# Optimization experiments

Hardware: AMD Instinct MI355X
Metric: run time of the kernel (lower is better)

Reference implementation:

```python
import jax, jax.numpy as jnp
import numpy as np

N = 100000        # num_nodes
E = 3200000       # num_edges
IN_C = 256        # in_channels (feature dim)
OUT_C = 128       # out_channels (embedding dim)
KAPPA = 0.95


def proj_norm_inf(W, kappa):
    """Row-wise projection of W onto the l-inf operator-norm ball of radius kappa:
    rows whose l1 norm exceeds kappa are projected (abs values onto the simplex
    of radius kappa via sort, signs restored). Matches projection_norm_inf."""
    a = jnp.abs(W)
    s = jnp.sign(W)
    rowsum = a.sum(axis=-1)                      # [rows]
    n = W.shape[-1]
    u = jnp.sort(a, axis=-1)[:, ::-1]            # descending
    css = jnp.cumsum(u, axis=-1) - kappa
    ind = jnp.arange(1, n + 1, dtype=W.dtype)
    cond = (u - css / ind) > 0                   # prefix-true pattern
    rho = jnp.sum(cond, axis=-1)                 # number of active coords (>=1 when rowsum>kappa)
    rho_safe = jnp.maximum(rho, 1)
    theta = jnp.take_along_axis(css, (rho_safe - 1)[:, None], axis=-1)[:, 0] / rho_safe.astype(W.dtype)
    w_proj = jnp.maximum(a - theta[:, None], 0.0) * s
    return jnp.where((rowsum > kappa)[:, None], w_proj, W)


def gcn_conv(x, W, src, dst, num_nodes):
    """PyG GCNConv (bias=False, normalize=True, add_self_loops=True):
    out = D^{-1/2} (A + I) D^{-1/2} (x @ W.T)"""
    loop = jnp.arange(num_nodes, dtype=src.dtype)
    src_f = jnp.concatenate([src, loop])
    dst_f = jnp.concatenate([dst, loop])
    ones = jnp.ones(src_f.shape[0], dtype=x.dtype)
    deg = jax.ops.segment_sum(ones, dst_f, num_segments=num_nodes)   # [N]
    dinv = jnp.where(deg > 0, jax.lax.rsqrt(jnp.maximum(deg, 1.0)), 0.0)
    norm = dinv[src_f] * dinv[dst_f]                                 # [E+N]
    h = x @ W.T                                                      # [N, OUT_C]
    msg = h[src_f] * norm[:, None]                                   # gather + scale
    return jax.ops.segment_sum(msg, dst_f, num_segments=num_nodes)   # scatter-add


def setup_inputs() -> dict:
    key = jax.random.key(0)
    k1, k2, k3, k4, k5 = jax.random.split(key, 5)
    features = jax.random.normal(k1, (N, IN_C), dtype=jnp.float32)
    edge_index = jax.random.randint(k2, (2, E), 0, N, dtype=jnp.int32)
    embeddings = 0.01 * jax.random.uniform(k3, (N, OUT_C), dtype=jnp.float32)
    # xavier_uniform-ish init for weights
    lim_c = float(np.sqrt(6.0 / (OUT_C + OUT_C)))
    lim_m = float(np.sqrt(6.0 / (IN_C + OUT_C)))
    W_conv = jax.random.uniform(k4, (OUT_C, OUT_C), dtype=jnp.float32, minval=-lim_c, maxval=lim_c)
    W_mlp = jax.random.uniform(k5, (OUT_C, IN_C), dtype=jnp.float32, minval=-lim_m, maxval=lim_m)
    return {"features": features, "edge_index": edge_index, "embeddings": embeddings,
            "W_conv": W_conv, "W_mlp": W_mlp}


def reference(features, edge_index, embeddings, W_conv, W_mlp):
    # SoftIGNN.forward: project conv weight, then one IGNN layer:
    # x = relu(GCNConv(embeddings, edge_index) + Linear(features))
    W_p = proj_norm_inf(W_conv, KAPPA)
    src, dst = edge_index[0], edge_index[1]
    agg = gcn_conv(embeddings, W_p, src, dst, N)     # [N, OUT_C]
    x = agg + features @ W_mlp.T                     # [N, OUT_C]
    return jax.nn.relu(x)
```

## Files before the change

kernel.cpp:

```cpp
#include <hip/hip_runtime.h>

#define KAPPA 0.95f

typedef __attribute__((ext_vector_type(8))) short short8;
typedef __attribute__((ext_vector_type(4))) float f32x4;
typedef __attribute__((ext_vector_type(2))) float f32x2;

static __device__ inline unsigned short f2bf(float f) {
    unsigned int u = __float_as_uint(f);
    unsigned int rounding = 0x7fffu + ((u >> 16) & 1u);
    u += rounding;
    return (unsigned short)(u >> 16);
}
static __device__ inline unsigned int pack2bf(float x, float y) {
    return (unsigned int)f2bf(x) | ((unsigned int)f2bf(y) << 16);
}

#define H_SCALE 4096.0f

__global__ __launch_bounds__(128) void proj_kernel(const float* __restrict__ W,
                                                   unsigned short* __restrict__ Wp_bf) {
    const int r = blockIdx.x;
    const int tid = threadIdx.x;
    __shared__ float s[128];
    __shared__ float c[128];
    __shared__ int rho_s;

    const float w = W[r * 128 + tid];
    const float a = fabsf(w);
    s[tid] = a;
    if (tid == 0) rho_s = 0;
    __syncthreads();

    for (int k = 2; k <= 128; k <<= 1) {
        for (int j = k >> 1; j > 0; j >>= 1) {
            int ixj = tid ^ j;
            if (ixj > tid) {
                bool up = ((tid & k) == 0);
                float x = s[tid], y = s[ixj];
                if ((x > y) == up) { s[tid] = y; s[ixj] = x; }
            }
            __syncthreads();
        }
    }

    const float u = s[127 - tid];
    c[tid] = u;
    __syncthreads();
    for (int off = 1; off < 128; off <<= 1) {
        float add = (tid >= off) ? c[tid - off] : 0.f;
        __syncthreads();
        c[tid] += add;
        __syncthreads();
    }
    const float rowsum = c[127];
    const float css = c[tid] - KAPPA;
    if (u - css / (float)(tid + 1) > 0.f) atomicAdd(&rho_s, 1);
    __syncthreads();

    float out = w;
    if (rowsum > KAPPA) {
        int rho = max(rho_s, 1);
        float theta = (c[rho - 1] - KAPPA) / (float)rho;
        float m = fmaxf(a - theta, 0.f);
        out = (w > 0.f) ? m : ((w < 0.f) ? -m : 0.f);
    }
    Wp_bf[r * 128 + tid] = f2bf(out);
}

__global__ void convw_kernel(const float* __restrict__ Wm, unsigned short* __restrict__ Wbf,
                             int n) {
    int i = blockIdx.x * blockDim.x + threadIdx.x;
    if (i < n) Wbf[i] = f2bf(Wm[i]);
}

__global__ __launch_bounds__(256) void rhist_kernel(const int* __restrict__ dst,
                                                    int* __restrict__ l2c, int E, unsigned N,
                                                    int chunk) {
    __shared__ int hist[512];
    const int b = blockIdx.x;
    const int i0 = b * chunk;
    const int i1 = min(i0 + chunk, E);
    for (int t = threadIdx.x; t < 512; t += 256) hist[t] = 0;
    __syncthreads();
    for (int i = i0 + threadIdx.x; i < i1; i += 256) {
        unsigned g = ((unsigned)dst[i] * 512u) / N;
        atomicAdd(&hist[g], 1);
    }
    __syncthreads();
    for (int t = threadIdx.x; t < 512; t += 256) l2c[(t << 9) | b] = hist[t];
}

__global__ __launch_bounds__(256) void rsum_kernel(const int* __restrict__ l2c,
                                                   int* __restrict__ R) {
    __shared__ int tmp[256];
    const int g = blockIdx.x;
    int s = 0;
    for (int j = threadIdx.x; j < 512; j += 256) s += l2c[(g << 9) | j];
    tmp[threadIdx.x] = s;
    __syncthreads();
    for (int off = 128; off > 0; off >>= 1) {
        if (threadIdx.x < off) tmp[threadIdx.x] += tmp[threadIdx.x + off];
        __syncthreads();
    }
    if (threadIdx.x == 0) R[g] = tmp[0];
}

__global__ __launch_bounds__(512) void rscan_kernel(const int* __restrict__ R,
                                                    int* __restrict__ Gbase) {
    __shared__ int tmp[512];
    const int tid = threadIdx.x;
    int v = R[tid];
    tmp[tid] = v;
    __syncthreads();
    int val = v;
    for (int off = 1; off < 512; off <<= 1) {
        int add = (tid >= off) ? tmp[tid - off] : 0;
        __syncthreads();
        val += add;
        tmp[tid] = val;
        __syncthreads();
    }
    Gbase[tid] = val - v;
}

__global__ __launch_bounds__(512) void rowscan_kernel(const int* __restrict__ l2c,
                                                      const int* __restrict__ Gbase,
                                                      int* __restrict__ l2base) {
    __shared__ int tmp[512];
    const int g = blockIdx.x;
    const int tid = threadIdx.x;
    int v = l2c[(g << 9) | tid];
    tmp[tid] = v;
    __syncthreads();
    int val = v;
    for (int off = 1; off < 512; off <<= 1) {
        int add = (tid >= off) ? tmp[tid - off] : 0;
        __syncthreads();
        val += add;
        tmp[tid] = val;
        __syncthreads();
    }
    l2base[(g << 9) | tid] = Gbase[g] + val - v;
}

__global__ __launch_bounds__(256) void rpart_kernel(const int* __restrict__ src,
                                                    const int* __restrict__ dst,
                                                    const int* __restrict__ l2base,
                                                    unsigned* __restrict__ queue2, int E,
                                                    unsigned N, int chunk) {
    __shared__ int base[512];
    const int b = blockIdx.x;
    const int i0 = b * chunk;
    const int i1 = min(i0 + chunk, E);
    for (int t = threadIdx.x; t < 512; t += 256) base[t] = l2base[(t << 9) | b];
    __syncthreads();
    for (int i = i0 + threadIdx.x; i < i1; i += 256) {
        unsigned d = (unsigned)dst[i];
        unsigned s = (unsigned)src[i];
        unsigned g = (d * 512u) / N;
        unsigned v0g = (g * N + 511u) >> 9;
        int p = atomicAdd(&base[g], 1);
        queue2[p] = ((d - v0g) << 24) | s;
    }
}

__global__ __launch_bounds__(1024) void subfill_kernel(const unsigned* __restrict__ queue2,
                                                       const int* __restrict__ Gbase,
                                                       int* __restrict__ csr_src,
                                                       int* __restrict__ counts,
                                                       int* __restrict__ cursor,
                                                       float* __restrict__ dinv, unsigned N,
                                                       int E) {
    __shared__ int cnt[256];
    __shared__ int ofs[256];
    __shared__ int stage[8192];
    const int B = blockIdx.x;
    const int g = (B & 7) * 64 + (B >> 3);
    const int e0 = Gbase[g];
    const int e1 = (g == 511) ? E : Gbase[g + 1];
    const unsigned v0 = ((unsigned)g * N + 511u) >> 9;
    const unsigned v1 = min((((unsigned)g + 1u) * N + 511u) >> 9, N);
    const int nn = (int)(v1 - v0);
    const int tid = threadIdx.x;
    if (tid < 256) cnt[tid] = 0;
    __syncthreads();
    for (int i = e0 + tid; i < e1; i += 1024) atomicAdd(&cnt[queue2[i] >> 24], 1);
    __syncthreads();
    if (tid < 256) ofs[tid] = cnt[tid];
    __syncthreads();
    for (int off = 1; off < 256; off <<= 1) {
        int add = (tid < 256 && tid >= off) ? ofs[tid - off] : 0;
        __syncthreads();
        if (tid < 256) ofs[tid] += add;
        __syncthreads();
    }
    if (tid < nn) {
        int excl = ofs[tid] - cnt[tid];
        counts[v0 + tid] = cnt[tid];
        cursor[v0 + tid] = e0 + excl;
        dinv[v0 + tid] = rsqrtf((float)(cnt[tid] + 1));
    }
    __syncthreads();
    if (tid < 256) ofs[tid] -= cnt[tid];
    __syncthreads();
    for (int i = e0 + tid; i < e1; i += 1024) {
        unsigned raw = queue2[i];
        int p = atomicAdd(&ofs[raw >> 24], 1);
        stage[p] = (int)(raw & 0xFFFFFFu);
    }
    __syncthreads();
    const int tot = e1 - e0;
    for (int t = tid; t < tot; t += 1024) csr_src[e0 + t] = stage[t];
}

template <int KD, int MODE>
__global__ __launch_bounds__(512) void gemm_mfma(const float* __restrict__ X,
                                                 const unsigned short* __restrict__ Wbf,
                                                 const float* __restrict__ dinv,
                                                 const float* ADD,
                                                 unsigned int* __restrict__ out_u32,
                                                 float* out_f, int nrows) {
    __shared__ __align__(16) unsigned short ldsW[128 * KD];
    const int tid = threadIdx.x;
    const int w = tid >> 6;
    const int l = tid & 63;
    const int l16 = l & 15;
    const int kg = l >> 4;
    const unsigned swz = (unsigned)((l16 & 7) << 4);
    const int row0 = blockIdx.x * 128;
    const int row = row0 + w * 16 + l16;
    const int rload = min(row, nrows - 1);
    const float* xrow = X + (size_t)rload * KD + kg * 8;

    {
        const uint4* wsrc = reinterpret_cast<const uint4*>(Wbf);
        char* lb = reinterpret_cast<char*>(ldsW);
        constexpr int NCH = 128 * KD / 8;
#pragma unroll
        for (int i = 0; i < NCH / 512; ++i) {
            int idx = i * 512 + tid;
            int sidx = idx * 8;
            unsigned byte = (unsigned)(sidx * 2);
            byte ^= (unsigned)(((sidx / KD) & 7) << 4);
            *reinterpret_cast<uint4*>(lb + byte) = wsrc[idx];
        }
    }
    __syncthreads();

    f32x4 acc[8];
#pragma unroll
    for (int j = 0; j < 8; ++j) acc[j] = (f32x4)(0.f);

    const char* lbr = reinterpret_cast<const char*>(ldsW);
    constexpr int NT = KD / 32;
#pragma unroll
    for (int t = 0; t < NT; ++t) {
        const float4 v0 = *reinterpret_cast<const float4*>(xrow + t * 32);
        const float4 v1 = *reinterpret_cast<const float4*>(xrow + t * 32 + 4);
        union { uint4 u; short8 s; } cvt;
        cvt.u.x = pack2bf(v0.x, v0.y);
        cvt.u.y = pack2bf(v0.z, v0.w);
        cvt.u.z = pack2bf(v1.x, v1.y);
        cvt.u.w = pack2bf(v1.z, v1.w);
        const short8 a = cvt.s;
#pragma unroll
        for (int ct = 0; ct < 8; ++ct) {
            const int c = ct * 16 + l16;
            unsigned byte = (unsigned)((c * KD + t * 32 + kg * 8) * 2) ^ swz;
            short8 wv = *reinterpret_cast<const short8*>(lbr + byte);
            acc[ct] = __builtin_amdgcn_mfma_f32_16x16x32_bf16(wv, a, acc[ct], 0, 0, 0);
        }
    }

    if (row < nrows) {
        if (MODE == 0) {
            const float dv = dinv[row] * H_SCALE;
#pragma unroll
            for (int ct = 0; ct < 8; ++ct) {
                f32x4 d = acc[ct];
                unsigned lo = __builtin_amdgcn_cvt_pk_fp8_f32(d[0] * dv, d[1] * dv, 0u, false);
                unsigned hi = __builtin_amdgcn_cvt_pk_fp8_f32(d[2] * dv, d[3] * dv, lo, true);
                out_u32[(size_t)row * 32 + ct * 4 + kg] = hi;
            }
        } else {
#pragma unroll
            for (int ct = 0; ct < 8; ++ct) {
                f32x4 d = acc[ct];
                const float4 a =
                    *reinterpret_cast<const float4*>(&ADD[(size_t)row * 128 + ct * 16 + kg * 4]);
                float4 o;
                o.x = fmaxf(d[0] + a.x, 0.f);
                o.y = fmaxf(d[1] + a.y, 0.f);
                o.z = fmaxf(d[2] + a.z, 0.f);
                o.w = fmaxf(d[3] + a.w, 0.f);
                *reinterpret_cast<float4*>(&out_f[(size_t)row * 128 + ct * 16 + kg * 4]) = o;
            }
        }
    }
}

static __device__ inline void unp8v(f32x2* acc, unsigned wv, int off) {
    acc[off + 0] += __builtin_amdgcn_cvt_pk_f32_fp8(wv, false);
    acc[off + 1] += __builtin_amdgcn_cvt_pk_f32_fp8(wv, true);
}
static __device__ inline void unp16(f32x2* acc, uint4 val) {
    unp8v(acc, val.x, 0);
    unp8v(acc, val.y, 2);
    unp8v(acc, val.z, 4);
    unp8v(acc, val.w, 6);
}

__global__ __launch_bounds__(256) void agg_kernel(const uint4* __restrict__ h8,
                                                  const int* __restrict__ csr_src,
                                                  const int* __restrict__ cursor,
                                                  const int* __restrict__ counts,
                                                  const float* __restrict__ dinv,
                                                  float* __restrict__ agg, int n) {
    int v = blockIdx.x * 4 + (threadIdx.x >> 6);
    if (v >= n) return;
    const int lane = threadIdx.x & 63;
    const int eg = lane >> 3;
    const int c = lane & 7;
    const int cnt = counts[v];
    const int start = cursor[v];

    f32x2 acc[8];
#pragma unroll
    for (int j = 0; j < 8; ++j) acc[j] = (f32x2)(0.f);

    int i0 = (eg < cnt) ? csr_src[start + eg] : -1;
    int i1 = (8 + eg < cnt) ? csr_src[start + 8 + eg] : -1;
    for (int base = 0; base < cnt; base += 16) {
        int s0 = i0, s1 = i1;
        int n0 = base + 16 + eg;
        int n1 = base + 24 + eg;
        i0 = (n0 < cnt) ? csr_src[start + n0] : -1;
        i1 = (n1 < cnt) ? csr_src[start + n1] : -1;
        uint4 va, vb;
        if (s0 >= 0) va = h8[(size_t)s0 * 8 + c];
        if (s1 >= 0) vb = h8[(size_t)s1 * 8 + c];
        if (s0 >= 0) unp16(acc, va);
        if (s1 >= 0) unp16(acc, vb);
    }
    if (eg == 0) {
        uint4 val = h8[(size_t)v * 8 + c];
        unp16(acc, val);
    }
#pragma unroll
    for (int j = 0; j < 8; ++j) {
#pragma unroll
        for (int k = 0; k < 2; ++k) {
            acc[j][k] += __shfl_xor(acc[j][k], 8);
            acc[j][k] += __shfl_xor(acc[j][k], 16);
            acc[j][k] += __shfl_xor(acc[j][k], 32);
        }
    }
    if (eg == 0) {
        const float dv = dinv[v] * (1.0f / H_SCALE);
#pragma unroll
        for (int k = 0; k < 4; ++k) {
            float4 o = {acc[2 * k][0] * dv, acc[2 * k][1] * dv, acc[2 * k + 1][0] * dv,
                        acc[2 * k + 1][1] * dv};
            *reinterpret_cast<float4*>(&agg[(size_t)v * 128 + c * 16 + k * 4]) = o;
        }
    }
}

extern "C" void kernel_launch(void* const* d_in, const int* in_sizes, int n_in,
                              void* d_out, int out_size, void* d_ws, size_t ws_size,
                              hipStream_t stream) {
    const float* features = (const float*)d_in[0];
    const int*   edge     = (const int*)d_in[1];
    const float* emb      = (const float*)d_in[2];
    const float* Wconv    = (const float*)d_in[3];
    const float* Wmlp     = (const float*)d_in[4];
    float* out = (float*)d_out;

    const int N = in_sizes[0] / 256;
    const int E = in_sizes[1] / 2;
    const int* src = edge;
    const int* dst = edge + E;
    const int chunk = (E + 511) / 512;

    char* ws = (char*)d_ws;
    size_t o = 0;
    auto take = [&](size_t b) {
        size_t cur = o;
        o += (b + 255) & ~(size_t)255;
        return cur;
    };
    unsigned short* Wp_bf   = (unsigned short*)(ws + take((size_t)128 * 128 * 2));
    unsigned short* Wm_bf   = (unsigned short*)(ws + take((size_t)128 * 256 * 2));
    int*            counts  = (int*)(ws + take((size_t)N * 4));
    int*            cursor  = (int*)(ws + take((size_t)N * 4));
    float*          dinv    = (float*)(ws + take((size_t)N * 4));
    int*            l2c     = (int*)(ws + take((size_t)512 * 512 * 4));
    int*            l2base  = (int*)(ws + take((size_t)512 * 512 * 4));
    int*            R       = (int*)(ws + take((size_t)512 * 4));
    int*            Gbase   = (int*)(ws + take((size_t)512 * 4));
    int*            csr_src = (int*)(ws + take((size_t)E * 4));
    size_t qbytes = (size_t)E * 4;
    size_t hbytes = (size_t)N * 128;
    char*  qh     = ws + take(qbytes > hbytes ? qbytes : hbytes);
    unsigned*     queue2 = (unsigned*)qh;
    unsigned int* h8     = (unsigned int*)qh;
    (void)ws_size; (void)n_in; (void)out_size;

    hipLaunchKernelGGL(proj_kernel, dim3(128), dim3(128), 0, stream, Wconv, Wp_bf);
    hipLaunchKernelGGL(convw_kernel, dim3((128 * 256 + 255) / 256), dim3(256), 0, stream, Wmlp,
                       Wm_bf, 128 * 256);
    hipLaunchKernelGGL(rhist_kernel, dim3(512), dim3(256), 0, stream, dst, l2c, E, (unsigned)N,
                       chunk);
    hipLaunchKernelGGL(rsum_kernel, dim3(512), dim3(256), 0, stream, l2c, R);
    hipLaunchKernelGGL(rscan_kernel, dim3(1), dim3(512), 0, stream, R, Gbase);
    hipLaunchKernelGGL(rowscan_kernel, dim3(512), dim3(512), 0, stream, l2c, Gbase, l2base);
    hipLaunchKernelGGL(rpart_kernel, dim3(512), dim3(256), 0, stream, src, dst, l2base, queue2, E,
                       (unsigned)N, chunk);
    hipLaunchKernelGGL(subfill_kernel, dim3(512), dim3(1024), 0, stream, queue2, Gbase, csr_src,
                       counts, cursor, dinv, (unsigned)N, E);
    hipLaunchKernelGGL((gemm_mfma<128, 0>), dim3((N + 127) / 128), dim3(512), 0, stream, emb,
                       Wp_bf, dinv, (const float*)nullptr, h8, (float*)nullptr, N);
    hipLaunchKernelGGL(agg_kernel, dim3((N + 3) / 4), dim3(256), 0, stream, (const uint4*)h8,
                       csr_src, cursor, counts, dinv, out, N);
    hipLaunchKernelGGL((gemm_mfma<256, 1>), dim3((N + 127) / 128), dim3(512), 0, stream, features,
                       Wm_bf, (const float*)nullptr, out, (unsigned int*)nullptr, out, N);
}
```

Measured before the change: 206.4 us.

## Fuse scan kernels, store aggregation in bf16, deepen gather unroll

Merges the single-block global scan into the per-row scan kernel so each block recomputes the prefix of R, which removes one launch and the Gbase buffer. The aggregation kernel now writes bf16 output to a separate buffer instead of fp32 into out, and the final GEMM reads that bf16 buffer, halving the intermediate traffic at some precision cost. The gather loop processes four edge groups per iteration instead of two to raise memory-level parallelism, at the cost of more registers.

```diff
diff --git a/kernel.cpp b/kernel.cpp
--- a/kernel.cpp
+++ b/kernel.cpp
@@ -15,6 +15,8 @@
 static __device__ inline unsigned int pack2bf(float x, float y) {
     return (unsigned int)f2bf(x) | ((unsigned int)f2bf(y) << 16);
 }
+static __device__ inline float bflo(unsigned int u) { return __uint_as_float(u << 16); }
+static __device__ inline float bfhi(unsigned int u) { return __uint_as_float(u & 0xffff0000u); }
 
 #define H_SCALE 4096.0f
 
@@ -106,11 +108,23 @@
     if (threadIdx.x == 0) R[g] = tmp[0];
 }
 
-__global__ __launch_bounds__(512) void rscan_kernel(const int* __restrict__ R,
-                                                    int* __restrict__ Gbase) {
+__global__ __launch_bounds__(512) void rowscan_kernel(const int* __restrict__ l2c,
+                                                      const int* __restrict__ R,
+                                                      int* __restrict__ l2base) {
+    __shared__ int tmpR[512];
     __shared__ int tmp[512];
+    const int g = blockIdx.x;
     const int tid = threadIdx.x;
-    int v = R[tid];
+    tmpR[tid] = R[tid];
+    __syncthreads();
+    for (int off = 1; off < 512; off <<= 1) {
+        int add = (tid >= off) ? tmpR[tid - off] : 0;
+        __syncthreads();
+        tmpR[tid] += add;
+        __syncthreads();
+    }
+    const int gbase = (g == 0) ? 0 : tmpR[g - 1];
+    int v = l2c[(g << 9) | tid];
     tmp[tid] = v;
     __syncthreads();
     int val = v;
@@ -121,27 +135,7 @@
         tmp[tid] = val;
         __syncthreads();
     }
-    Gbase[tid] = val - v;
-}
-
-__global__ __launch_bounds__(512) void rowscan_kernel(const int* __restrict__ l2c,
-                                                      const int* __restrict__ Gbase,
-                                                      int* __restrict__ l2base) {
-    __shared__ int tmp[512];
-    const int g = blockIdx.x;
-    const int tid = threadIdx.x;
-    int v = l2c[(g << 9) | tid];
-    tmp[tid] = v;
-    __syncthreads();
-    int val = v;
-    for (int off = 1; off < 512; off <<= 1) {
-        int add = (tid >= off) ? tmp[tid - off] : 0;
-        __syncthreads();
-        val += add;
-        tmp[tid] = val;
-        __syncthreads();
-    }
-    l2base[(g << 9) | tid] = Gbase[g] + val - v;
+    l2base[(g << 9) | tid] = gbase + val - v;
 }
 
 __global__ __launch_bounds__(256) void rpart_kernel(const int* __restrict__ src,
@@ -166,7 +160,7 @@
 }
 
 __global__ __launch_bounds__(1024) void subfill_kernel(const unsigned* __restrict__ queue2,
-                                                       const int* __restrict__ Gbase,
+                                                       const int* __restrict__ l2base,
                                                        int* __restrict__ csr_src,
                                                        int* __restrict__ counts,
                                                        int* __restrict__ cursor,
@@ -177,8 +171,8 @@
     __shared__ int stage[8192];
     const int B = blockIdx.x;
     const int g = (B & 7) * 64 + (B >> 3);
-    const int e0 = Gbase[g];
-    const int e1 = (g == 511) ? E : Gbase[g + 1];
+    const int e0 = l2base[g << 9];
+    const int e1 = (g == 511) ? E : l2base[(g + 1) << 9];
     const unsigned v0 = ((unsigned)g * N + 511u) >> 9;
     const unsigned v1 = min((((unsigned)g + 1u) * N + 511u) >> 9, N);
     const int nn = (int)(v1 - v0);
@@ -218,7 +212,7 @@
 __global__ __launch_bounds__(512) void gemm_mfma(const float* __restrict__ X,
                                                  const unsigned short* __restrict__ Wbf,
                                                  const float* __restrict__ dinv,
-                                                 const float* ADD,
+                                                 const unsigned int* __restrict__ ADDbf,
                                                  unsigned int* __restrict__ out_u32,
                                                  float* out_f, int nrows) {
     __shared__ __align__(16) unsigned short ldsW[128 * KD];
@@ -287,13 +281,13 @@
 #pragma unroll
             for (int ct = 0; ct < 8; ++ct) {
                 f32x4 d = acc[ct];
-                const float4 a =
-                    *reinterpret_cast<const float4*>(&ADD[(size_t)row * 128 + ct * 16 + kg * 4]);
+                const uint2 ab =
+                    *reinterpret_cast<const uint2*>(&ADDbf[(size_t)row * 64 + ct * 8 + kg * 2]);
                 float4 o;
-                o.x = fmaxf(d[0] + a.x, 0.f);
-                o.y = fmaxf(d[1] + a.y, 0.f);
-                o.z = fmaxf(d[2] + a.z, 0.f);
-                o.w = fmaxf(d[3] + a.w, 0.f);
+                o.x = fmaxf(d[0] + bflo(ab.x), 0.f);
+                o.y = fmaxf(d[1] + bfhi(ab.x), 0.f);
+                o.z = fmaxf(d[2] + bflo(ab.y), 0.f);
+                o.w = fmaxf(d[3] + bfhi(ab.y), 0.f);
                 *reinterpret_cast<float4*>(&out_f[(size_t)row * 128 + ct * 16 + kg * 4]) = o;
             }
         }
@@ -316,7 +310,7 @@
                                                   const int* __restrict__ cursor,
                                                   const int* __restrict__ counts,
                                                   const float* __restrict__ dinv,
-                                                  float* __restrict__ agg, int n) {
+                                                  unsigned int* __restrict__ aggbf, int n) {
     int v = blockIdx.x * 4 + (threadIdx.x >> 6);
     if (v >= n) return;
     const int lane = threadIdx.x & 63;
@@ -331,17 +325,24 @@
 
     int i0 = (eg < cnt) ? csr_src[start + eg] : -1;
     int i1 = (8 + eg < cnt) ? csr_src[start + 8 + eg] : -1;
-    for (int base = 0; base < cnt; base += 16) {
-        int s0 = i0, s1 = i1;
-        int n0 = base + 16 + eg;
-        int n1 = base + 24 + eg;
+    int i2 = (16 + eg < cnt) ? csr_src[start + 16 + eg] : -1;
+    int i3 = (24 + eg < cnt) ? csr_src[start + 24 + eg] : -1;
+    for (int base = 0; base < cnt; base += 32) {
+        int s0 = i0, s1 = i1, s2 = i2, s3 = i3;
+        int n0 = base + 32 + eg, n1 = n0 + 8, n2 = n0 + 16, n3 = n0 + 24;
         i0 = (n0 < cnt) ? csr_src[start + n0] : -1;
         i1 = (n1 < cnt) ? csr_src[start + n1] : -1;
-        uint4 va, vb;
+        i2 = (n2 < cnt) ? csr_src[start + n2] : -1;
+        i3 = (n3 < cnt) ? csr_src[start + n3] : -1;
+        uint4 va, vb, vc, vd;
         if (s0 >= 0) va = h8[(size_t)s0 * 8 + c];
         if (s1 >= 0) vb = h8[(size_t)s1 * 8 + c];
+        if (s2 >= 0) vc = h8[(size_t)s2 * 8 + c];
+        if (s3 >= 0) vd = h8[(size_t)s3 * 8 + c];
         if (s0 >= 0) unp16(acc, va);
         if (s1 >= 0) unp16(acc, vb);
+        if (s2 >= 0) unp16(acc, vc);
+        if (s3 >= 0) unp16(acc, vd);
     }
     if (eg == 0) {
         uint4 val = h8[(size_t)v * 8 + c];
@@ -358,12 +359,17 @@
     }
     if (eg == 0) {
         const float dv = dinv[v] * (1.0f / H_SCALE);
-#pragma unroll
-        for (int k = 0; k < 4; ++k) {
-            float4 o = {acc[2 * k][0] * dv, acc[2 * k][1] * dv, acc[2 * k + 1][0] * dv,
-                        acc[2 * k + 1][1] * dv};
-            *reinterpret_cast<float4*>(&agg[(size_t)v * 128 + c * 16 + k * 4]) = o;
-        }
+        uint4 o0, o1;
+        o0.x = pack2bf(acc[0][0] * dv, acc[0][1] * dv);
+        o0.y = pack2bf(acc[1][0] * dv, acc[1][1] * dv);
+        o0.z = pack2bf(acc[2][0] * dv, acc[2][1] * dv);
+        o0.w = pack2bf(acc[3][0] * dv, acc[3][1] * dv);
+        o1.x = pack2bf(acc[4][0] * dv, acc[4][1] * dv);
+        o1.y = pack2bf(acc[5][0] * dv, acc[5][1] * dv);
+        o1.z = pack2bf(acc[6][0] * dv, acc[6][1] * dv);
+        o1.w = pack2bf(acc[7][0] * dv, acc[7][1] * dv);
+        *reinterpret_cast<uint4*>(&aggbf[(size_t)v * 64 + c * 8]) = o0;
+        *reinterpret_cast<uint4*>(&aggbf[(size_t)v * 64 + c * 8 + 4]) = o1;
     }
 }
 
@@ -398,8 +404,8 @@
     int*            l2c     = (int*)(ws + take((size_t)512 * 512 * 4));
     int*            l2base  = (int*)(ws + take((size_t)512 * 512 * 4));
     int*            R       = (int*)(ws + take((size_t)512 * 4));
-    int*            Gbase   = (int*)(ws + take((size_t)512 * 4));
     int*            csr_src = (int*)(ws + take((size_t)E * 4));
+    unsigned int*   aggbf   = (unsigned int*)(ws + take((size_t)N * 128 * 2));
     size_t qbytes = (size_t)E * 4;
     size_t hbytes = (size_t)N * 128;
     char*  qh     = ws + take(qbytes > hbytes ? qbytes : hbytes);
@@ -413,16 +419,15 @@
     hipLaunchKernelGGL(rhist_kernel, dim3(512), dim3(256), 0, stream, dst, l2c, E, (unsigned)N,
                        chunk);
     hipLaunchKernelGGL(rsum_kernel, dim3(512), dim3(256), 0, stream, l2c, R);
-    hipLaunchKernelGGL(rscan_kernel, dim3(1), dim3(512), 0, stream, R, Gbase);
-    hipLaunchKernelGGL(rowscan_kernel, dim3(512), dim3(512), 0, stream, l2c, Gbase, l2base);
+    hipLaunchKernelGGL(rowscan_kernel, dim3(512), dim3(512), 0, stream, l2c, R, l2base);
     hipLaunchKernelGGL(rpart_kernel, dim3(512), dim3(256), 0, stream, src, dst, l2base, queue2, E,
                        (unsigned)N, chunk);
-    hipLaunchKernelGGL(subfill_kernel, dim3(512), dim3(1024), 0, stream, queue2, Gbase, csr_src,
+    hipLaunchKernelGGL(subfill_kernel, dim3(512), dim3(1024), 0, stream, queue2, l2base, csr_src,
                        counts, cursor, dinv, (unsigned)N, E);
     hipLaunchKernelGGL((gemm_mfma<128, 0>), dim3((N + 127) / 128), dim3(512), 0, stream, emb,
-                       Wp_bf, dinv, (const float*)nullptr, h8, (float*)nullptr, N);
+                       Wp_bf, dinv, (const unsigned int*)nullptr, h8, (float*)nullptr, N);
     hipLaunchKernelGGL(agg_kernel, dim3((N + 3) / 4), dim3(256), 0, stream, (const uint4*)h8,
-                       csr_src, cursor, counts, dinv, out, N);
+                       csr_src, cursor, counts, dinv, aggbf, N);
     hipLaunchKernelGGL((gemm_mfma<256, 1>), dim3((N + 127) / 128), dim3(512), 0, stream, features,
-                       Wm_bf, (const float*)nullptr, out, (unsigned int*)nullptr, out, N);
-}
+                       Wm_bf, (const float*)nullptr, aggbf, (unsigned int*)nullptr, out, N);
+}
```

After: 218.4 us. 5.8% more time.
